# Kernel tuning notes

Measured on AMD Instinct MI355X. Metric: run time of the kernel, lower is better.

Reference implementation:

```python
import jax, jax.numpy as jnp
import numpy as np

DIM = 1024
HEADS = 8
DIM_HEAD = 64
DIM_INNER = HEADS * DIM_HEAD  # 512


def setup_inputs() -> dict:
    key = jax.random.key(0)
    k1, k2, k3, k4 = jax.random.split(key, 4)
    x = jax.random.normal(k1, (1, 4096, DIM), dtype=jnp.float32)
    gamma = jnp.ones((DIM,), dtype=jnp.float32)
    w_qkv = jax.random.normal(k2, (DIM, 3 * DIM_INNER), dtype=jnp.float32) * (DIM ** -0.5)
    w_out = jax.random.normal(k3, (DIM_INNER, DIM), dtype=jnp.float32) * (DIM_INNER ** -0.5)
    return {"x": x, "gamma": gamma, "w_qkv": w_qkv, "w_out": w_out}


def _rmsnorm(x, gamma):
    # F.normalize(x, dim=-1) * sqrt(dim) * gamma
    norm = jnp.sqrt(jnp.sum(x * x, axis=-1, keepdims=True))
    x = x / jnp.maximum(norm, 1e-12)
    return x * (DIM ** 0.5) * gamma


def reference(x, gamma, w_qkv, w_out):
    b, n, _ = x.shape
    h, d = HEADS, DIM_HEAD
    normed = _rmsnorm(x, gamma)
    qkv = normed @ w_qkv  # [b, n, 3*h*d]
    qkv = qkv.reshape(b, n, 3, h, d)
    q = jnp.transpose(qkv[:, :, 0], (0, 2, 1, 3))  # b h n d
    k = jnp.transpose(qkv[:, :, 1], (0, 2, 1, 3))
    v = jnp.transpose(qkv[:, :, 2], (0, 2, 1, 3))
    # default_attention (faithful: scales q by d**0.5 as in source)
    q = q * (d ** 0.5)
    sim = jnp.einsum('bhid,bhjd->bhij', q, k)
    mask_value = -jnp.finfo(sim.dtype).max
    causal_mask = jnp.triu(jnp.ones((n, n), dtype=bool), 1)
    sim = jnp.where(causal_mask, mask_value, sim)
    attn = jax.nn.softmax(sim, axis=-1)
    out = jnp.einsum('bhij,bhjd->bhid', attn, v)  # b h n d
    out = jnp.transpose(out, (0, 2, 1, 3)).reshape(b, n, h * d)
    return out @ w_out  # [b, n, dim]
```

## Files before the change

kernel.cpp:

```cpp
#include <hip/hip_runtime.h>
#include <math.h>

#define SEQ 4096
#define DIM 1024
#define HEADS 8
#define DINNER 512
#define QKVW 1536
#define PAD 80
#define CHUNK 16

typedef unsigned short u16;
typedef __attribute__((ext_vector_type(8))) short s8v;
typedef __attribute__((ext_vector_type(4))) float f4v;
#define MFMA(a, b, c) __builtin_amdgcn_mfma_f32_16x16x32_bf16(a, b, c, 0, 0, 0)

__device__ __forceinline__ u16 f2bf(float f) {
    unsigned u = __float_as_uint(f);
    u += 0x7fff + ((u >> 16) & 1);
    return (u16)(u >> 16);
}
__device__ __forceinline__ float bf2f(u16 b) { return __uint_as_float(((unsigned)b) << 16); }

__device__ __forceinline__ void gload16(const u16* g, u16* l) {
    __builtin_amdgcn_global_load_lds(
        (const __attribute__((address_space(1))) unsigned int*)g,
        (__attribute__((address_space(3))) unsigned int*)l, 16, 0, 0);
}

__device__ __forceinline__ int base16(int qt) {
    int a = qt >> 4, b = qt & 15;
    return 8 * a * (a + 1) + b * (a + 1);
}
__device__ __forceinline__ float* po_sel(int T, float* pd, float* pw) {
    return (T < 1024) ? pd + (size_t)T * 4096 : pw + (size_t)(T - 1024) * 4096;
}

__global__ __launch_bounds__(256) void rmsnorm_split(const float* __restrict__ x,
                                                     const float* __restrict__ gamma,
                                                     u16* __restrict__ hi,
                                                     u16* __restrict__ lo) {
    __shared__ float red[4];
    const int row = blockIdx.x, t = threadIdx.x;
    const float* xr = x + (size_t)row * DIM;
    float v[4];
    float ss = 0.f;
#pragma unroll
    for (int i = 0; i < 4; ++i) { v[i] = xr[t + i * 256]; ss += v[i] * v[i]; }
#pragma unroll
    for (int off = 32; off >= 1; off >>= 1) ss += __shfl_xor(ss, off, 64);
    if ((t & 63) == 0) red[t >> 6] = ss;
    __syncthreads();
    float scale = 32.0f / fmaxf(sqrtf(red[0] + red[1] + red[2] + red[3]), 1e-12f);
#pragma unroll
    for (int i = 0; i < 4; ++i) {
        int c = t + i * 256;
        float y = v[i] * scale * gamma[c];
        u16 h = f2bf(y);
        hi[(size_t)row * DIM + c] = h;
        lo[(size_t)row * DIM + c] = f2bf(y - bf2f(h));
    }
}

__global__ __launch_bounds__(256) void transpose_split(const float* __restrict__ in,
                                                       u16* __restrict__ hi,
                                                       u16* __restrict__ lo,
                                                       int R, int C, int want_lo) {
    __shared__ float tile[64][65];
    const int c0 = blockIdx.x * 64, r0 = blockIdx.y * 64;
    const int t = threadIdx.x, col = t & 63, rb = t >> 6;
#pragma unroll
    for (int j = 0; j < 16; ++j)
        tile[rb + j * 4][col] = in[(size_t)(r0 + rb + j * 4) * C + c0 + col];
    __syncthreads();
#pragma unroll
    for (int j = 0; j < 16; ++j) {
        int cc = rb + j * 4;
        float v = tile[col][cc];
        size_t oi = (size_t)(c0 + cc) * R + r0 + col;
        u16 h = f2bf(v);
        hi[oi] = h;
        if (want_lo) lo[oi] = f2bf(v - bf2f(h));
    }
}

__global__ __launch_bounds__(256) void gemm_qkv_128(
    const u16* __restrict__ Ah, const u16* __restrict__ Al,
    const u16* __restrict__ Bh, const u16* __restrict__ Bl,
    u16* __restrict__ qh, u16* __restrict__ ql,
    u16* __restrict__ kh, u16* __restrict__ kl, u16* __restrict__ vtp) {
    __shared__ __align__(16) u16 AsH[128 * 64], AsL[128 * 64];
    __shared__ __align__(16) u16 BsH[64 * 64], BsL[64 * 64];
    const int t = threadIdx.x;
    const int bn = blockIdx.x * 64, bm = blockIdx.y * 128;
    const int w = t >> 6, lane = t & 63, m = lane & 15, q = lane >> 4;
    const int wr = w >> 1, wc = w & 1;
    f4v acc[4][2];
#pragma unroll
    for (int i = 0; i < 4; ++i)
#pragma unroll
        for (int j = 0; j < 2; ++j) acc[i][j] = (f4v){0.f, 0.f, 0.f, 0.f};

    for (int k0 = 0; k0 < DIM; k0 += 64) {
        __syncthreads();
#pragma unroll
        for (int i = 0; i < 4; ++i) {
            int idx0 = i * 256 + w * 64;
            int row = (idx0 + lane) >> 3;
            int col = ((lane & 7) * 8) ^ ((row & 7) * 8);
            gload16(&Ah[(size_t)(bm + row) * DIM + k0 + col], &AsH[idx0 * 8]);
            gload16(&Al[(size_t)(bm + row) * DIM + k0 + col], &AsL[idx0 * 8]);
            if (i < 2) {
                gload16(&Bh[(size_t)(bn + row) * DIM + k0 + col], &BsH[idx0 * 8]);
                gload16(&Bl[(size_t)(bn + row) * DIM + k0 + col], &BsL[idx0 * 8]);
            }
        }
        __syncthreads();
#pragma unroll
        for (int kk = 0; kk < 64; kk += 32) {
            s8v a_h[4], a_l[4], b_h[2], b_l[2];
#pragma unroll
            for (int f = 0; f < 4; ++f) {
                int ar = wr * 64 + f * 16 + m;
                int ab = ar * 128 + (((kk + q * 8) * 2) ^ ((ar & 7) << 4));
                a_h[f] = *(const s8v*)((const char*)AsH + ab);
                a_l[f] = *(const s8v*)((const char*)AsL + ab);
            }
#pragma unroll
            for (int f = 0; f < 2; ++f) {
                int br = wc * 32 + f * 16 + m;
                int bb = br * 128 + (((kk + q * 8) * 2) ^ ((br & 7) << 4));
                b_h[f] = *(const s8v*)((const char*)BsH + bb);
                b_l[f] = *(const s8v*)((const char*)BsL + bb);
            }
#pragma unroll
            for (int fm = 0; fm < 4; ++fm)
#pragma unroll
                for (int fn = 0; fn < 2; ++fn) {
                    acc[fm][fn] = MFMA(a_h[fm], b_h[fn], acc[fm][fn]);
                    acc[fm][fn] = MFMA(a_l[fm], b_h[fn], acc[fm][fn]);
                    acc[fm][fn] = MFMA(a_h[fm], b_l[fn], acc[fm][fn]);
                }
        }
    }
    const int region = bn >> 9;
#pragma unroll
    for (int fm = 0; fm < 4; ++fm)
#pragma unroll
        for (int fn = 0; fn < 2; ++fn)
#pragma unroll
            for (int r = 0; r < 4; ++r) {
                int gr = bm + wr * 64 + fm * 16 + q * 4 + r;
                int gc = bn + wc * 32 + fn * 16 + m;
                float v = acc[fm][fn][r];
                if (region == 0) {
                    v *= 8.0f;
                    u16 h = f2bf(v);
                    qh[(size_t)gr * DINNER + gc] = h;
                    ql[(size_t)gr * DINNER + gc] = f2bf(v - bf2f(h));
                } else if (region == 1) {
                    u16 h = f2bf(v);
                    kh[(size_t)gr * DINNER + (gc - 512)] = h;
                    kl[(size_t)gr * DINNER + (gc - 512)] = f2bf(v - bf2f(h));
                } else {
                    vtp[(size_t)(gc - 1024) * SEQ + gr] = f2bf(v);
                }
            }
}

__global__ __launch_bounds__(256) void attn_chunk(
    const u16* __restrict__ qhp, const u16* __restrict__ qlp,
    const u16* __restrict__ kh, const u16* __restrict__ kl,
    const u16* __restrict__ vt,
    float* __restrict__ po_dout, float* __restrict__ po_wqt,
    float* __restrict__ ml) {
    __shared__ __align__(16) u16 KH[2][64 * 64], KL[2][64 * 64], VT[2][64 * 64];
    const int t = threadIdx.x;
    const int bx = blockIdx.x;
    const int qt = 63 - (bx >> 2), c = bx & 3, h = blockIdx.y;
    if (c * CHUNK > qt) return;
    const int kt0 = c * CHUNK;
    const int kt1 = (qt < kt0 + CHUNK - 1) ? qt : (kt0 + CHUNK - 1);
    const int w = t >> 6, lane = t & 63, m = lane & 15, g = lane >> 4;

    const size_t qrow = (size_t)(qt * 64 + w * 16 + m) * DINNER + h * 64;
    const s8v qf_h0 = *(const s8v*)&qhp[qrow + g * 8];
    const s8v qf_h1 = *(const s8v*)&qhp[qrow + 32 + g * 8];
    const s8v qf_l0 = *(const s8v*)&qlp[qrow + g * 8];
    const s8v qf_l1 = *(const s8v*)&qlp[qrow + 32 + g * 8];

    const int sg0a = w * 64, sg0b = 256 + w * 64;
    const int srowa = (sg0a + lane) >> 3, srowb = (sg0b + lane) >> 3;
    const int sca = ((lane & 7) ^ (srowa & 7)) * 8;
    const int scb = ((lane & 7) ^ (srowb & 7)) * 8;

    f4v o[4] = {{0.f, 0.f, 0.f, 0.f}, {0.f, 0.f, 0.f, 0.f},
                {0.f, 0.f, 0.f, 0.f}, {0.f, 0.f, 0.f, 0.f}};
    float mi_s = -1e30f, li_s = 0.f;

    {
        const u16* kr = &kh[(size_t)(kt0 * 64) * DINNER + h * 64];
        const u16* lr = &kl[(size_t)(kt0 * 64) * DINNER + h * 64];
        const u16* vr = &vt[(size_t)(h * 64) * SEQ + kt0 * 64];
        gload16(kr + (size_t)srowa * DINNER + sca, &KH[0][sg0a * 8]);
        gload16(kr + (size_t)srowb * DINNER + scb, &KH[0][sg0b * 8]);
        gload16(lr + (size_t)srowa * DINNER + sca, &KL[0][sg0a * 8]);
        gload16(lr + (size_t)srowb * DINNER + scb, &KL[0][sg0b * 8]);
        gload16(vr + (size_t)srowa * SEQ + sca, &VT[0][sg0a * 8]);
        gload16(vr + (size_t)srowb * SEQ + scb, &VT[0][sg0b * 8]);
    }
    __syncthreads();

    int cur = 0;
    for (int kt = kt0; kt <= kt1; ++kt) {
        if (kt < kt1) {
            int nb = cur ^ 1;
            const u16* kr = &kh[(size_t)((kt + 1) * 64) * DINNER + h * 64];
            const u16* lr = &kl[(size_t)((kt + 1) * 64) * DINNER + h * 64];
            const u16* vr = &vt[(size_t)(h * 64) * SEQ + (kt + 1) * 64];
            gload16(kr + (size_t)srowa * DINNER + sca, &KH[nb][sg0a * 8]);
            gload16(kr + (size_t)srowb * DINNER + scb, &KH[nb][sg0b * 8]);
            gload16(lr + (size_t)srowa * DINNER + sca, &KL[nb][sg0a * 8]);
            gload16(lr + (size_t)srowb * DINNER + scb, &KL[nb][sg0b * 8]);
            gload16(vr + (size_t)srowa * SEQ + sca, &VT[nb][sg0a * 8]);
            gload16(vr + (size_t)srowb * SEQ + scb, &VT[nb][sg0b * 8]);
        }

        const char* KHc = (const char*)KH[cur];
        const char* KLc = (const char*)KL[cur];
        f4v s[4] = {{0.f, 0.f, 0.f, 0.f}, {0.f, 0.f, 0.f, 0.f},
                    {0.f, 0.f, 0.f, 0.f}, {0.f, 0.f, 0.f, 0.f}};
#pragma unroll
        for (int ct = 0; ct < 4; ++ct) {
            int rr = ct * 16 + m, rb = rr * 128, sw = (rr & 7) << 4;
            s8v bh0 = *(const s8v*)(KHc + rb + ((g * 16) ^ sw));
            s8v bl0 = *(const s8v*)(KLc + rb + ((g * 16) ^ sw));
            s[ct] = MFMA(bh0, qf_h0, s[ct]);
            s[ct] = MFMA(bh0, qf_l0, s[ct]);
            s[ct] = MFMA(bl0, qf_h0, s[ct]);
            s8v bh1 = *(const s8v*)(KHc + rb + ((64 + g * 16) ^ sw));
            s8v bl1 = *(const s8v*)(KLc + rb + ((64 + g * 16) ^ sw));
            s[ct] = MFMA(bh1, qf_h1, s[ct]);
            s[ct] = MFMA(bh1, qf_l1, s[ct]);
            s[ct] = MFMA(bl1, qf_h1, s[ct]);
        }
        if (kt == qt) {
#pragma unroll
            for (int ct = 0; ct < 4; ++ct)
#pragma unroll
                for (int r = 0; r < 4; ++r)
                    if (ct * 16 + g * 4 + r > w * 16 + m) s[ct][r] = -1e30f;
        }

        float rm = -1e30f;
#pragma unroll
        for (int ct = 0; ct < 4; ++ct)
#pragma unroll
            for (int r = 0; r < 4; ++r) rm = fmaxf(rm, s[ct][r]);
        rm = fmaxf(rm, __shfl_xor(rm, 16, 64));
        rm = fmaxf(rm, __shfl_xor(rm, 32, 64));
        float mn = fmaxf(mi_s, rm);
        float al = __expf(mi_s - mn);
        mi_s = mn;
        float rs = 0.f;
#pragma unroll
        for (int ct = 0; ct < 4; ++ct)
#pragma unroll
            for (int r = 0; r < 4; ++r) {
                s[ct][r] = __expf(s[ct][r] - mn);
                rs += s[ct][r];
            }
        rs += __shfl_xor(rs, 16, 64);
        rs += __shfl_xor(rs, 32, 64);
        li_s = li_s * al + rs;
        float alo[4];
#pragma unroll
        for (int r = 0; r < 4; ++r) alo[r] = __shfl(al, g * 4 + r, 64);

        __syncthreads();

        const int pr = w * 16 + m, pb = pr * 128, psw = (pr & 7) << 4;
#pragma unroll
        for (int ct = 0; ct < 4; ++ct) {
            unsigned w0 = (unsigned)f2bf(s[ct][0]) | ((unsigned)f2bf(s[ct][1]) << 16);
            unsigned w1 = (unsigned)f2bf(s[ct][2]) | ((unsigned)f2bf(s[ct][3]) << 16);
            *(uint2*)((char*)KH[cur] + pb + ((ct * 32 + g * 8) ^ psw)) = make_uint2(w0, w1);
        }
#pragma unroll
        for (int ct = 0; ct < 4; ++ct)
#pragma unroll
            for (int r = 0; r < 4; ++r) o[ct][r] *= alo[r];
#pragma unroll
        for (int kk = 0; kk < 2; ++kk) {
            s8v ap = *(const s8v*)((const char*)KH[cur] + pb + ((kk * 64 + g * 16) ^ psw));
#pragma unroll
            for (int ct = 0; ct < 4; ++ct) {
                int vr2 = ct * 16 + m;
                s8v bv = *(const s8v*)((const char*)VT[cur] + vr2 * 128 +
                                       ((kk * 64 + g * 16) ^ ((vr2 & 7) << 4)));
                o[ct] = MFMA(ap, bv, o[ct]);
            }
        }
        __syncthreads();
        cur ^= 1;
    }

    const int T = h * 160 + base16(qt) + c;
    float* po = po_sel(T, po_dout, po_wqt);
#pragma unroll
    for (int ct = 0; ct < 4; ++ct)
#pragma unroll
        for (int r = 0; r < 4; ++r)
            po[(size_t)(w * 16 + g * 4 + r) * 64 + ct * 16 + m] = o[ct][r];
    if (g == 0) {
        ml[(size_t)T * 128 + w * 16 + m] = mi_s;
        ml[(size_t)T * 128 + 64 + w * 16 + m] = li_s;
    }
}

__global__ __launch_bounds__(256) void attn_merge(
    float* __restrict__ po_dout, float* __restrict__ po_wqt,
    const float* __restrict__ ml, u16* __restrict__ atto) {
    const int qt = blockIdx.x, h = blockIdx.y;
    const int nc = (qt >> 4) + 1;
    const int t = threadIdx.x, col = t & 63, rg = t >> 6;
    const int T0 = h * 160 + base16(qt);
    for (int j = 0; j < 16; ++j) {
        int row = rg * 16 + j;
        float mv[4], lv[4], M = -1e30f;
#pragma unroll 4
        for (int cc = 0; cc < 4; ++cc)
            if (cc < nc) {
                mv[cc] = ml[(size_t)(T0 + cc) * 128 + row];
                lv[cc] = ml[(size_t)(T0 + cc) * 128 + 64 + row];
                M = fmaxf(M, mv[cc]);
            }
        float acc = 0.f, den = 0.f;
#pragma unroll 4
        for (int cc = 0; cc < 4; ++cc)
            if (cc < nc) {
                const float* po = po_sel(T0 + cc, po_dout, po_wqt);
                float wg = __expf(mv[cc] - M);
                den += lv[cc] * wg;
                acc += wg * po[(size_t)row * 64 + col];
            }
        atto[(size_t)(qt * 64 + row) * DINNER + h * 64 + col] = f2bf(acc / den);
    }
}

__global__ __launch_bounds__(256) void attn_mfma(
    const u16* __restrict__ qh, const u16* __restrict__ ql,
    const u16* __restrict__ kh, const u16* __restrict__ kl,
    const u16* __restrict__ vt, u16* __restrict__ atto) {
    __shared__ u16 Qh[64 * PAD], Ql[64 * PAD], KP[64 * PAD], Kl[64 * PAD], Vt[64 * PAD];
    const int t = threadIdx.x;
    const int qt = blockIdx.x, h = blockIdx.y;
    const int w = t >> 6, lane = t & 63, m = lane & 15, q = lane >> 4;

#pragma unroll
    for (int i = 0; i < 2; ++i) {
        int c = t + i * 256, row = c >> 3, ch = (c & 7) * 8;
        *(uint4*)&Qh[row * PAD + ch] =
            *(const uint4*)&qh[(size_t)(qt * 64 + row) * DINNER + h * 64 + ch];
        *(uint4*)&Ql[row * PAD + ch] =
            *(const uint4*)&ql[(size_t)(qt * 64 + row) * DINNER + h * 64 + ch];
    }

    f4v o[4] = {{0.f, 0.f, 0.f, 0.f}, {0.f, 0.f, 0.f, 0.f},
                {0.f, 0.f, 0.f, 0.f}, {0.f, 0.f, 0.f, 0.f}};
    float mi[4] = {-1e30f, -1e30f, -1e30f, -1e30f};
    float li[4] = {0.f, 0.f, 0.f, 0.f};

    for (int kt = 0; kt <= qt; ++kt) {
        __syncthreads();
#pragma unroll
        for (int i = 0; i < 2; ++i) {
            int c = t + i * 256, row = c >> 3, ch = (c & 7) * 8;
            *(uint4*)&KP[row * PAD + ch] =
                *(const uint4*)&kh[(size_t)(kt * 64 + row) * DINNER + h * 64 + ch];
            *(uint4*)&Kl[row * PAD + ch] =
                *(const uint4*)&kl[(size_t)(kt * 64 + row) * DINNER + h * 64 + ch];
            *(uint4*)&Vt[row * PAD + ch] =
                *(const uint4*)&vt[(size_t)(h * 64 + row) * SEQ + kt * 64 + ch];
        }
        __syncthreads();

        f4v s[4] = {{0.f, 0.f, 0.f, 0.f}, {0.f, 0.f, 0.f, 0.f},
                    {0.f, 0.f, 0.f, 0.f}, {0.f, 0.f, 0.f, 0.f}};
#pragma unroll
        for (int kk = 0; kk < 64; kk += 32) {
            s8v ah = *(const s8v*)&Qh[(w * 16 + m) * PAD + kk + q * 8];
            s8v al = *(const s8v*)&Ql[(w * 16 + m) * PAD + kk + q * 8];
#pragma unroll
            for (int ct = 0; ct < 4; ++ct) {
                s8v bh = *(const s8v*)&KP[(ct * 16 + m) * PAD + kk + q * 8];
                s8v bl = *(const s8v*)&Kl[(ct * 16 + m) * PAD + kk + q * 8];
                s[ct] = MFMA(ah, bh, s[ct]);
                s[ct] = MFMA(al, bh, s[ct]);
                s[ct] = MFMA(ah, bl, s[ct]);
            }
        }
        if (kt == qt) {
#pragma unroll
            for (int ct = 0; ct < 4; ++ct)
#pragma unroll
                for (int r = 0; r < 4; ++r)
                    if (ct * 16 + m > w * 16 + q * 4 + r) s[ct][r] = -1e30f;
        }

        float alpha[4];
#pragma unroll
        for (int r = 0; r < 4; ++r) {
            float rm = fmaxf(fmaxf(s[0][r], s[1][r]), fmaxf(s[2][r], s[3][r]));
#pragma unroll
            for (int off = 8; off >= 1; off >>= 1) rm = fmaxf(rm, __shfl_xor(rm, off, 64));
            float mn = fmaxf(mi[r], rm);
            alpha[r] = __expf(mi[r] - mn);
            mi[r] = mn;
            float rs = 0.f;
#pragma unroll
            for (int ct = 0; ct < 4; ++ct) {
                s[ct][r] = __expf(s[ct][r] - mn);
                rs += s[ct][r];
            }
#pragma unroll
            for (int off = 8; off >= 1; off >>= 1) rs += __shfl_xor(rs, off, 64);
            li[r] = li[r] * alpha[r] + rs;
        }

        __syncthreads();
#pragma unroll
        for (int ct = 0; ct < 4; ++ct)
#pragma unroll
            for (int r = 0; r < 4; ++r) {
                KP[(w * 16 + q * 4 + r) * PAD + ct * 16 + m] = f2bf(s[ct][r]);
                o[ct][r] *= alpha[r];
            }
#pragma unroll
        for (int kk = 0; kk < 64; kk += 32) {
            s8v ap = *(const s8v*)&KP[(w * 16 + m) * PAD + kk + q * 8];
#pragma unroll
            for (int ct = 0; ct < 4; ++ct) {
                s8v bv = *(const s8v*)&Vt[(ct * 16 + m) * PAD + kk + q * 8];
                o[ct] = MFMA(ap, bv, o[ct]);
            }
        }
    }

#pragma unroll
    for (int r = 0; r < 4; ++r) {
        float inv = 1.0f / li[r];
#pragma unroll
        for (int ct = 0; ct < 4; ++ct)
            atto[(size_t)(qt * 64 + w * 16 + q * 4 + r) * DINNER + h * 64 + ct * 16 + m] =
                f2bf(o[ct][r] * inv);
    }
}

__global__ __launch_bounds__(256) void gemm_out_bf16(const u16* __restrict__ A,
                                                     const u16* __restrict__ Bt,
                                                     float* __restrict__ C) {
    __shared__ u16 As[64 * PAD], Bs[64 * PAD];
    const int t = threadIdx.x;
    const int bn = blockIdx.x * 64, bm = blockIdx.y * 64;
    const int w = t >> 6, lane = t & 63, m = lane & 15, q = lane >> 4;
    f4v acc[4] = {{0.f, 0.f, 0.f, 0.f}, {0.f, 0.f, 0.f, 0.f},
                  {0.f, 0.f, 0.f, 0.f}, {0.f, 0.f, 0.f, 0.f}};
    for (int k0 = 0; k0 < DINNER; k0 += 64) {
        __syncthreads();
#pragma unroll
        for (int i = 0; i < 2; ++i) {
            int c = t + i * 256, row = c >> 3, ch = (c & 7) * 8;
            *(uint4*)&As[row * PAD + ch] = *(const uint4*)&A[(size_t)(bm + row) * DINNER + k0 + ch];
            *(uint4*)&Bs[row * PAD + ch] = *(const uint4*)&Bt[(size_t)(bn + row) * DINNER + k0 + ch];
        }
        __syncthreads();
#pragma unroll
        for (int kk = 0; kk < 64; kk += 32) {
            s8v a = *(const s8v*)&As[(w * 16 + m) * PAD + kk + q * 8];
#pragma unroll
            for (int ct = 0; ct < 4; ++ct) {
                s8v b = *(const s8v*)&Bs[(ct * 16 + m) * PAD + kk + q * 8];
                acc[ct] = MFMA(a, b, acc[ct]);
            }
        }
    }
#pragma unroll
    for (int ct = 0; ct < 4; ++ct)
#pragma unroll
        for (int r = 0; r < 4; ++r)
            C[(size_t)(bm + w * 16 + q * 4 + r) * DIM + bn + ct * 16 + m] = acc[ct][r];
}

extern "C" void kernel_launch(void* const* d_in, const int* in_sizes, int n_in,
                              void* d_out, int out_size, void* d_ws, size_t ws_size,
                              hipStream_t stream) {
    const float* x     = (const float*)d_in[0];
    const float* gamma = (const float*)d_in[1];
    const float* w_qkv = (const float*)d_in[2];
    const float* w_out = (const float*)d_in[3];
    float* out = (float*)d_out;

    u16* nh = (u16*)d_out;
    u16* nl = nh + (size_t)SEQ * DIM;

    u16* p = (u16*)d_ws;
    u16* wqt_h = p; p += (size_t)QKVW * DIM;
    u16* wqt_l = p; p += (size_t)QKVW * DIM;
    u16* wot   = p; p += (size_t)DIM * DINNER;
    u16* qh = p; p += (size_t)SEQ * DINNER;
    u16* ql = p; p += (size_t)SEQ * DINNER;
    u16* kh = p; p += (size_t)SEQ * DINNER;
    u16* kl = p; p += (size_t)SEQ * DINNER;
    u16* vt = p; p += (size_t)DINNER * SEQ;
    u16* atto = p; p += (size_t)SEQ * DINNER;

    float* po_dout = (float*)d_out;
    float* po_wqt  = (float*)wqt_h;
    float* ml      = (float*)p;
    const size_t need = (size_t)((char*)(ml + (size_t)1280 * 128) - (char*)d_ws);
    const bool split = ws_size >= need;

    transpose_split<<<dim3(QKVW / 64, DIM / 64), 256, 0, stream>>>(w_qkv, wqt_h, wqt_l,
                                                                   DIM, QKVW, 1);
    transpose_split<<<dim3(DIM / 64, DINNER / 64), 256, 0, stream>>>(w_out, wot, nullptr,
                                                                     DINNER, DIM, 0);
    rmsnorm_split<<<SEQ, 256, 0, stream>>>(x, gamma, nh, nl);
    gemm_qkv_128<<<dim3(QKVW / 64, SEQ / 128), 256, 0, stream>>>(nh, nl, wqt_h, wqt_l,
                                                                 qh, ql, kh, kl, vt);
    if (split) {
        attn_chunk<<<dim3(256, HEADS), 256, 0, stream>>>(qh, ql, kh, kl, vt,
                                                         po_dout, po_wqt, ml);
        attn_merge<<<dim3(SEQ / 64, HEADS), 256, 0, stream>>>(po_dout, po_wqt, ml, atto);
    } else {
        attn_mfma<<<dim3(SEQ / 64, HEADS), 256, 0, stream>>>(qh, ql, kh, kl, vt, atto);
    }
    gemm_out_bf16<<<dim3(DIM / 64, SEQ / 64), 256, 0, stream>>>(atto, wot, out);
}
```

Measured before the change: 293.9 us.

## Enlarge output GEMM tile with swizzled direct-to-LDS loads; vectorize rmsnorm

```diff
diff --git a/kernel.cpp b/kernel.cpp
--- a/kernel.cpp
+++ b/kernel.cpp
@@ -41,24 +41,26 @@
                                                      u16* __restrict__ lo) {
     __shared__ float red[4];
     const int row = blockIdx.x, t = threadIdx.x;
-    const float* xr = x + (size_t)row * DIM;
-    float v[4];
-    float ss = 0.f;
-#pragma unroll
-    for (int i = 0; i < 4; ++i) { v[i] = xr[t + i * 256]; ss += v[i] * v[i]; }
+    const float4 xv = ((const float4*)(x + (size_t)row * DIM))[t];
+    float ss = xv.x * xv.x + xv.y * xv.y + xv.z * xv.z + xv.w * xv.w;
 #pragma unroll
     for (int off = 32; off >= 1; off >>= 1) ss += __shfl_xor(ss, off, 64);
     if ((t & 63) == 0) red[t >> 6] = ss;
     __syncthreads();
     float scale = 32.0f / fmaxf(sqrtf(red[0] + red[1] + red[2] + red[3]), 1e-12f);
-#pragma unroll
-    for (int i = 0; i < 4; ++i) {
-        int c = t + i * 256;
-        float y = v[i] * scale * gamma[c];
-        u16 h = f2bf(y);
-        hi[(size_t)row * DIM + c] = h;
-        lo[(size_t)row * DIM + c] = f2bf(y - bf2f(h));
-    }
+    const float4 gv = ((const float4*)gamma)[t];
+    float y[4] = {xv.x * scale * gv.x, xv.y * scale * gv.y,
+                  xv.z * scale * gv.z, xv.w * scale * gv.w};
+    unsigned hw0, hw1, lw0, lw1;
+    {
+        u16 h0 = f2bf(y[0]), h1 = f2bf(y[1]), h2 = f2bf(y[2]), h3 = f2bf(y[3]);
+        hw0 = (unsigned)h0 | ((unsigned)h1 << 16);
+        hw1 = (unsigned)h2 | ((unsigned)h3 << 16);
+        lw0 = (unsigned)f2bf(y[0] - bf2f(h0)) | ((unsigned)f2bf(y[1] - bf2f(h1)) << 16);
+        lw1 = (unsigned)f2bf(y[2] - bf2f(h2)) | ((unsigned)f2bf(y[3] - bf2f(h3)) << 16);
+    }
+    *(uint2*)&hi[(size_t)row * DIM + t * 4] = make_uint2(hw0, hw1);
+    *(uint2*)&lo[(size_t)row * DIM + t * 4] = make_uint2(lw0, lw1);
 }
 
 __global__ __launch_bounds__(256) void transpose_split(const float* __restrict__ in,
@@ -456,39 +458,62 @@
     }
 }
 
-__global__ __launch_bounds__(256) void gemm_out_bf16(const u16* __restrict__ A,
-                                                     const u16* __restrict__ Bt,
-                                                     float* __restrict__ C) {
-    __shared__ u16 As[64 * PAD], Bs[64 * PAD];
+__global__ __launch_bounds__(256) void gemm_out_128(const u16* __restrict__ A,
+                                                    const u16* __restrict__ Bt,
+                                                    float* __restrict__ C) {
+    __shared__ __align__(16) u16 As[128 * 64], Bs[64 * 64];
     const int t = threadIdx.x;
-    const int bn = blockIdx.x * 64, bm = blockIdx.y * 64;
+    const int bn = blockIdx.x * 64, bm = blockIdx.y * 128;
     const int w = t >> 6, lane = t & 63, m = lane & 15, q = lane >> 4;
-    f4v acc[4] = {{0.f, 0.f, 0.f, 0.f}, {0.f, 0.f, 0.f, 0.f},
-                  {0.f, 0.f, 0.f, 0.f}, {0.f, 0.f, 0.f, 0.f}};
+    const int wr = w >> 1, wc = w & 1;
+    f4v acc[4][2];
+#pragma unroll
+    for (int i = 0; i < 4; ++i)
+#pragma unroll
+        for (int j = 0; j < 2; ++j) acc[i][j] = (f4v){0.f, 0.f, 0.f, 0.f};
+
     for (int k0 = 0; k0 < DINNER; k0 += 64) {
         __syncthreads();
 #pragma unroll
-        for (int i = 0; i < 2; ++i) {
-            int c = t + i * 256, row = c >> 3, ch = (c & 7) * 8;
-            *(uint4*)&As[row * PAD + ch] = *(const uint4*)&A[(size_t)(bm + row) * DINNER + k0 + ch];
-            *(uint4*)&Bs[row * PAD + ch] = *(const uint4*)&Bt[(size_t)(bn + row) * DINNER + k0 + ch];
+        for (int i = 0; i < 4; ++i) {
+            int idx0 = i * 256 + w * 64;
+            int row = (idx0 + lane) >> 3;
+            int col = ((lane & 7) * 8) ^ ((row & 7) * 8);
+            gload16(&A[(size_t)(bm + row) * DINNER + k0 + col], &As[idx0 * 8]);
+            if (i < 2)
+                gload16(&Bt[(size_t)(bn + row) * DINNER + k0 + col], &Bs[idx0 * 8]);
         }
         __syncthreads();
 #pragma unroll
         for (int kk = 0; kk < 64; kk += 32) {
-            s8v a = *(const s8v*)&As[(w * 16 + m) * PAD + kk + q * 8];
-#pragma unroll
-            for (int ct = 0; ct < 4; ++ct) {
-                s8v b = *(const s8v*)&Bs[(ct * 16 + m) * PAD + kk + q * 8];
-                acc[ct] = MFMA(a, b, acc[ct]);
-            }
-        }
-    }
-#pragma unroll
-    for (int ct = 0; ct < 4; ++ct)
-#pragma unroll
-        for (int r = 0; r < 4; ++r)
-            C[(size_t)(bm + w * 16 + q * 4 + r) * DIM + bn + ct * 16 + m] = acc[ct][r];
+            s8v a_f[4], b_f[2];
+#pragma unroll
+            for (int f = 0; f < 4; ++f) {
+                int ar = wr * 64 + f * 16 + m;
+                a_f[f] = *(const s8v*)((const char*)As + ar * 128 +
+                                       (((kk + q * 8) * 2) ^ ((ar & 7) << 4)));
+            }
+#pragma unroll
+            for (int f = 0; f < 2; ++f) {
+                int br = wc * 32 + f * 16 + m;
+                b_f[f] = *(const s8v*)((const char*)Bs + br * 128 +
+                                       (((kk + q * 8) * 2) ^ ((br & 7) << 4)));
+            }
+#pragma unroll
+            for (int fm = 0; fm < 4; ++fm)
+#pragma unroll
+                for (int fn = 0; fn < 2; ++fn)
+                    acc[fm][fn] = MFMA(a_f[fm], b_f[fn], acc[fm][fn]);
+        }
+    }
+#pragma unroll
+    for (int fm = 0; fm < 4; ++fm)
+#pragma unroll
+        for (int fn = 0; fn < 2; ++fn)
+#pragma unroll
+            for (int r = 0; r < 4; ++r)
+                C[(size_t)(bm + wr * 64 + fm * 16 + q * 4 + r) * DIM +
+                  bn + wc * 32 + fn * 16 + m] = acc[fm][fn][r];
 }
 
 extern "C" void kernel_launch(void* const* d_in, const int* in_sizes, int n_in,
@@ -534,5 +559,5 @@
     } else {
         attn_mfma<<<dim3(SEQ / 64, HEADS), 256, 0, stream>>>(qh, ql, kh, kl, vt, atto);
     }
-    gemm_out_bf16<<<dim3(DIM / 64, SEQ / 64), 256, 0, stream>>>(atto, wot, out);
-}
+    gemm_out_128<<<dim3(DIM / 64, SEQ / 128), 256, 0, stream>>>(atto, wot, out);
+}
```

After: 289.2 us. No clear change (-1.6%).
